# Kernel tuning notes

Measured on AMD Instinct MI355X. Metric: run time of the kernel, lower is better.

## Reference

```python
import jax, jax.numpy as jnp
import numpy as np

V, B, T, D, L, H = 32000, 2, 2048, 1024, 4, 16
HD = D // H            # 64
HID = int(2 * D * 4 / 3)  # 2730 (SwiGLU hidden, computed in BinaryMLP)
EPS = 1e-6


def setup_inputs() -> dict:
    key = jax.random.key(0)
    ks = jax.random.split(key, 16)
    s = 0.02
    return {
        'emb': jax.random.normal(ks[0], (V, D), jnp.float32) * s,
        'Wq':  jax.random.normal(ks[1], (L, D, D), jnp.float32) * s,
        'Wk':  jax.random.normal(ks[2], (L, D, D), jnp.float32) * s,
        'Wv':  jax.random.normal(ks[3], (L, D, D), jnp.float32) * s,
        'Wo':  jax.random.normal(ks[4], (L, D, D), jnp.float32) * s,
        'W1':  jax.random.normal(ks[5], (L, HID, D), jnp.float32) * s,
        'W3':  jax.random.normal(ks[6], (L, HID, D), jnp.float32) * s,
        'W2':  jax.random.normal(ks[7], (L, D, HID), jnp.float32) * s,
        'g1':  jnp.ones((L, D), jnp.float32),
        'g2':  jnp.ones((L, D), jnp.float32),
        'gf':  jnp.ones((D,), jnp.float32),
        'Wlm': jax.random.normal(ks[8], (V, D), jnp.float32) * s,
        'idx': jax.random.randint(ks[9], (B, T), 0, V, jnp.int64),
    }


def bitnet_quant(w):
    # BitNet b1.58: gamma = mean(|W|); ternarize then rescale (STE: identity grad)
    gamma = jnp.maximum(jnp.mean(jnp.abs(w)), 1e-5)
    wq = jnp.clip(jnp.round(w / gamma), -1.0, 1.0) * gamma
    return w + jax.lax.stop_gradient(wq - w)


def rmsnorm(x, g):
    return x * jax.lax.rsqrt(jnp.mean(x * x, axis=-1, keepdims=True) + EPS) * g


def rope_tables(t_len):
    inv_freq = 1.0 / (10000.0 ** (jnp.arange(0, HD, 2, dtype=jnp.float32) / HD))
    t = jnp.arange(t_len, dtype=jnp.float32)
    freqs = jnp.einsum('i,j->ij', t, inv_freq)       # [T, HD/2]
    emb = jnp.concatenate([freqs, freqs], axis=-1)    # [T, HD]
    return jnp.cos(emb), jnp.sin(emb)


def rotate_half(x):
    x1, x2 = x[..., : HD // 2], x[..., HD // 2:]
    return jnp.concatenate([-x2, x1], axis=-1)


def forward(emb, Wq, Wk, Wv, Wo, W1, W2, W3, g1, g2, gf, Wlm, idx):
    x = emb[idx]                                      # [B,T,D]
    cos, sin = rope_tables(T)                         # [T,HD]
    cos = cos[None, None]; sin = sin[None, None]      # [1,1,T,HD]
    causal = jnp.tril(jnp.ones((T, T), bool))[None, None]
    scale = 1.0 / np.sqrt(HD)

    for l in range(L):
        # --- attention ---
        h = rmsnorm(x, g1[l])
        q = jnp.einsum('btd,ed->bte', h, bitnet_quant(Wq[l]))
        k = jnp.einsum('btd,ed->bte', h, bitnet_quant(Wk[l]))
        v = jnp.einsum('btd,ed->bte', h, bitnet_quant(Wv[l]))
        q = q.reshape(B, T, H, HD).transpose(0, 2, 1, 3)  # [B,H,T,HD]
        k = k.reshape(B, T, H, HD).transpose(0, 2, 1, 3)
        v = v.reshape(B, T, H, HD).transpose(0, 2, 1, 3)
        q = q * cos + rotate_half(q) * sin
        k = k * cos + rotate_half(k) * sin
        att = jnp.einsum('bhqd,bhkd->bhqk', q, k) * scale
        att = jnp.where(causal, att, -jnp.inf)
        att = jax.nn.softmax(att, axis=-1)
        y = jnp.einsum('bhqk,bhkd->bhqd', att, v)
        y = y.transpose(0, 2, 1, 3).reshape(B, T, D)
        y = jnp.einsum('btd,ed->bte', y, bitnet_quant(Wo[l]))
        x = x + y
        # --- SwiGLU MLP ---
        h = rmsnorm(x, g2[l])
        a = jnp.einsum('btd,hd->bth', h, bitnet_quant(W1[l]))
        b = jnp.einsum('btd,hd->bth', h, bitnet_quant(W3[l]))
        m = jnp.einsum('bth,dh->btd', jax.nn.silu(a) * b, bitnet_quant(W2[l]))
        x = x + m

    x = rmsnorm(x, gf)
    logits = jnp.einsum('btd,vd->btv', x, Wlm)        # lm_head is plain Linear
    return logits


def reference(emb, Wq, Wk, Wv, Wo, W1, W2, W3, g1, g2, gf, Wlm, idx):
    return forward(emb, Wq, Wk, Wv, Wo, W1, W2, W3, g1, g2, gf, Wlm, idx)
```

## Files before the change

kernel.cpp:

```cpp
#include <hip/hip_runtime.h>

#define TT   2048
#define BBB  2
#define DDD  1024
#define LLL  4
#define HHH  16
#define VVV  32000
#define HIDR 2730
#define HIDP 2816
#define MMM  (BBB*TT)

typedef __bf16 bf16x8 __attribute__((ext_vector_type(8)));
typedef float  f32x4  __attribute__((ext_vector_type(4)));

#define BAR()    asm volatile("s_barrier" ::: "memory")
#define LGKM0()  asm volatile("s_waitcnt lgkmcnt(0)" ::: "memory")
#define VMC(n)   asm volatile("s_waitcnt vmcnt(" #n ")" ::: "memory")
#define SCHED0() __builtin_amdgcn_sched_barrier(0)

__device__ __forceinline__ void gl2lds16(const void* g, void* l) {
  __builtin_amdgcn_global_load_lds((const __attribute__((address_space(1))) void*)g,
                                   (__attribute__((address_space(3))) void*)l, 16, 0, 0);
}

__device__ __forceinline__ f32x4 mfma16(bf16x8 a, bf16x8 b, f32x4 c) {
  return __builtin_amdgcn_mfma_f32_16x16x32_bf16(a, b, c, 0, 0, 0);
}

__device__ __forceinline__ float block_reduce_sum(float v) {
  __shared__ float red[4];
  #pragma unroll
  for (int o = 32; o > 0; o >>= 1) v += __shfl_xor(v, o);
  int w = threadIdx.x >> 6;
  if ((threadIdx.x & 63) == 0) red[w] = v;
  __syncthreads();
  float r = red[0] + red[1] + red[2] + red[3];
  __syncthreads();
  return r;
}

struct QDesc { const float* src; __bf16* dst; int srcR, srcC, dstR, dstC, quant, rmul; };
struct QDescs { QDesc d[29]; };

__global__ __launch_bounds__(256) void reduce_abs_kernel(QDescs qd, float* partial) {
  const QDesc e = qd.d[blockIdx.y];
  size_t n4 = ((size_t)e.srcR * e.srcC) >> 2;
  const float4* s4 = (const float4*)e.src;
  float acc = 0.f;
  for (size_t i = (size_t)blockIdx.x * blockDim.x + threadIdx.x; i < n4;
       i += (size_t)gridDim.x * blockDim.x) {
    float4 v = s4[i];
    acc += fabsf(v.x) + fabsf(v.y) + fabsf(v.z) + fabsf(v.w);
  }
  float s = block_reduce_sum(acc);
  if (threadIdx.x == 0) partial[blockIdx.y * 256 + blockIdx.x] = s;
}

__global__ __launch_bounds__(256) void finalize_gamma_kernel(QDescs qd, const float* partial,
                                                             float* gamma) {
  int m = blockIdx.x;
  float v = partial[m * 256 + threadIdx.x];
  float s = block_reduce_sum(v);
  if (threadIdx.x == 0) {
    float n = (float)((size_t)qd.d[m].srcR * qd.d[m].srcC);
    gamma[m] = fmaxf(s / n, 1e-5f);
  }
}

__global__ __launch_bounds__(256) void quant_kernel(QDescs qd, const float* gamma) {
  const QDesc e = qd.d[blockIdx.y];
  float invg = 1.0f / gamma[blockIdx.y];
  int nc8 = e.dstC >> 3;
  for (int row = blockIdx.x; row < e.dstR; row += gridDim.x) {
    const float* srow = e.src + (size_t)row * e.srcC;
    bf16x8* drow = (bf16x8*)(e.dst + (size_t)row * e.rmul * e.dstC);
    bool rok = row < e.srcR;
    for (int c8 = threadIdx.x; c8 < nc8; c8 += 256) {
      int c = c8 * 8;
      float w[8];
      if (rok && c + 8 <= e.srcC) {
        float2 v01 = *(const float2*)(srow + c);
        float2 v23 = *(const float2*)(srow + c + 2);
        float2 v45 = *(const float2*)(srow + c + 4);
        float2 v67 = *(const float2*)(srow + c + 6);
        w[0] = v01.x; w[1] = v01.y; w[2] = v23.x; w[3] = v23.y;
        w[4] = v45.x; w[5] = v45.y; w[6] = v67.x; w[7] = v67.y;
      } else {
        #pragma unroll
        for (int j = 0; j < 8; ++j) w[j] = (rok && c + j < e.srcC) ? srow[c + j] : 0.f;
      }
      bf16x8 o;
      #pragma unroll
      for (int j = 0; j < 8; ++j) {
        if (e.quant) {
          float q = rintf(w[j] * invg);
          o[j] = (__bf16)fminf(1.f, fmaxf(-1.f, q));
        } else {
          o[j] = (__bf16)w[j];
        }
      }
      drow[c8] = o;
    }
  }
}

__global__ void rope_table_kernel(float* cosT, float* sinT) {
  int i = blockIdx.x * 256 + threadIdx.x;
  int t = i >> 5, j = i & 31;
  float inv = powf(10000.0f, -(float)j * (1.0f / 32.0f));
  float ang = (float)t * inv;
  cosT[i] = cosf(ang);
  sinT[i] = sinf(ang);
}

__global__ void idx_mode_kernel(const void* idxv, int* flag) {
  const long long* p = (const long long*)idxv;
  int good = 1;
  for (int i = threadIdx.x; i < (BBB * TT) / 2; i += 256) {
    long long v = p[i];
    if (v < 0 || v >= VVV) good = 0;
  }
  unsigned long long b = __ballot(good);
  __shared__ int r[4];
  if ((threadIdx.x & 63) == 0) r[threadIdx.x >> 6] = (b == ~0ULL) ? 1 : 0;
  __syncthreads();
  if (threadIdx.x == 0) flag[0] = r[0] & r[1] & r[2] & r[3];
}

__global__ __launch_bounds__(256) void gather_kernel(const float* emb, const void* idxv,
                                                     const int* flag, float* x) {
  int tok = blockIdx.x;
  long long id;
  if (flag[0]) id = ((const long long*)idxv)[tok];
  else         id = (long long)((const int*)idxv)[tok];
  const float4* src = (const float4*)(emb + (size_t)id * DDD);
  float4* dst = (float4*)(x + (size_t)tok * DDD);
  dst[threadIdx.x] = src[threadIdx.x];
}

__global__ __launch_bounds__(256) void rmsnorm_kernel(const float* x, const float* g, __bf16* h) {
  int tok = blockIdx.x;
  const float4* xr = (const float4*)(x + (size_t)tok * DDD);
  float4 v = xr[threadIdx.x];
  float ss = v.x * v.x + v.y * v.y + v.z * v.z + v.w * v.w;
  float tot = block_reduce_sum(ss);
  float r = rsqrtf(tot * (1.0f / (float)DDD) + 1e-6f);
  const float4* gr = (const float4*)g;
  float4 gv = gr[threadIdx.x];
  union { __bf16 o[4]; uint2 u2; } pk;
  pk.o[0] = (__bf16)(v.x * r * gv.x);
  pk.o[1] = (__bf16)(v.y * r * gv.y);
  pk.o[2] = (__bf16)(v.z * r * gv.z);
  pk.o[3] = (__bf16)(v.w * r * gv.w);
  *(uint2*)((char*)h + ((size_t)tok * DDD + threadIdx.x * 4) * 2) = pk.u2;
}

__global__ __launch_bounds__(256) void repack_kernel(const __bf16* qkv, const float* cosT,
                                                     const float* sinT, __bf16* Qp, __bf16* Kp,
                                                     __bf16* Vp) {
  int bh = blockIdx.y;
  int b = bh >> 4, h = bh & 15;
  int t0 = blockIdx.x * 64;
  int r = threadIdx.x >> 2;
  int cq = (threadIdx.x & 3) * 16;
  int t = t0 + r;
  __shared__ __bf16 vt[64][72];
  size_t src = ((size_t)b * TT + t) * 3072 + h * 64;

  #pragma unroll
  for (int which = 0; which < 2; ++which) {
    const __bf16* inp = qkv + (which ? 1024 : 0);
    __bf16* outp = which ? Kp : Qp;
    __bf16 val[16], par[16];
    *(bf16x8*)&val[0] = *(const bf16x8*)(inp + src + cq);
    *(bf16x8*)&val[8] = *(const bf16x8*)(inp + src + cq + 8);
    *(bf16x8*)&par[0] = *(const bf16x8*)(inp + src + (cq ^ 32));
    *(bf16x8*)&par[8] = *(const bf16x8*)(inp + src + (cq ^ 32) + 8);
    __bf16 o[16];
    #pragma unroll
    for (int i2 = 0; i2 < 16; ++i2) {
      int d = cq + i2;
      float c = cosT[t * 32 + (d & 31)];
      float s = sinT[t * 32 + (d & 31)];
      float x0 = (float)val[i2], xp = (float)par[i2];
      float res = (d < 32) ? (x0 * c - xp * s) : (x0 * c + xp * s);
      o[i2] = (__bf16)res;
    }
    *(bf16x8*)(outp + ((size_t)bh * TT + t) * 64 + cq) = *(bf16x8*)&o[0];
    *(bf16x8*)(outp + ((size_t)bh * TT + t) * 64 + cq + 8) = *(bf16x8*)&o[8];
  }

  bf16x8 v0 = *(const bf16x8*)(qkv + 2048 + src + cq);
  bf16x8 v1 = *(const bf16x8*)(qkv + 2048 + src + cq + 8);
  #pragma unroll
  for (int i2 = 0; i2 < 8; ++i2) {
    vt[r][cq + i2] = v0[i2];
    vt[r][cq + 8 + i2] = v1[i2];
  }
  __syncthreads();
  __bf16 ov[16];
  #pragma unroll
  for (int i2 = 0; i2 < 16; ++i2) ov[i2] = vt[cq + i2][r];
  *(bf16x8*)(Vp + ((size_t)bh * 64 + r) * TT + t0 + cq) = *(bf16x8*)&ov[0];
  *(bf16x8*)(Vp + ((size_t)bh * 64 + r) * TT + t0 + cq + 8) = *(bf16x8*)&ov[8];
}

__global__ __launch_bounds__(256) void attn_kernel(const __bf16* __restrict__ Qp,
                                                   const __bf16* __restrict__ Kp,
                                                   const __bf16* __restrict__ Vp,
                                                   __bf16* __restrict__ y) {
  int nwg = gridDim.x * gridDim.y;
  int orig = blockIdx.y * gridDim.x + blockIdx.x;
  int qq = nwg >> 3;
  int swz = (orig & 7) * qq + (orig >> 3);
  int qt = swz % gridDim.x, bh = swz / gridDim.x;

  int b = bh >> 4, h = bh & 15;
  int lane = threadIdx.x & 63, wave = threadIdx.x >> 6;
  int l15 = lane & 15, l4 = lane >> 4;
  int q0 = qt * 128;
  const int ssw = (l15 & 7);
  const int csw = ((lane & 7) ^ (lane >> 3)) * 8;
  const float SC = 0.125f * 1.44269504f;

  __shared__ __bf16 Ks[2][64 * 64];
  __shared__ __bf16 Vts[2][64 * 64];
  __shared__ __bf16 Ps[4][32 * 64];

  const __bf16* Qb = Qp + (size_t)bh * TT * 64;
  bf16x8 qf[2][2];
  #pragma unroll
  for (int mf = 0; mf < 2; ++mf)
    #pragma unroll
    for (int kk = 0; kk < 2; ++kk)
      qf[mf][kk] = *(const bf16x8*)(Qb + (size_t)(q0 + wave * 32 + mf * 16 + l15) * 64 +
                                    kk * 32 + l4 * 8);

  const f32x4 z4 = {0.f, 0.f, 0.f, 0.f};
  f32x4 acc[2][4];
  float mrow[2][4], lrow[2][4];
  #pragma unroll
  for (int mf = 0; mf < 2; ++mf)
    #pragma unroll
    for (int j = 0; j < 4; ++j) { mrow[mf][j] = -1e30f; lrow[mf][j] = 0.f; }
  #pragma unroll
  for (int mf = 0; mf < 2; ++mf)
    #pragma unroll
    for (int df = 0; df < 4; ++df) acc[mf][df] = z4;

  auto stage = [&](int kt, int buf) {
    int k0 = kt * 64;
    #pragma unroll
    for (int i = 0; i < 2; ++i) {
      int rbase = wave * 16 + i * 8;
      int row = rbase + (lane >> 3);
      gl2lds16(Kp + ((size_t)bh * TT + k0 + row) * 64 + csw, &Ks[buf][rbase * 64]);
      gl2lds16(Vp + ((size_t)bh * 64 + row) * TT + k0 + csw, &Vts[buf][rbase * 64]);
    }
  };

  int nkt = q0 / 64 + 2;
  stage(0, 0);
  __syncthreads();

  for (int kt = 0; kt < nkt; ++kt) {
    int k0 = kt * 64;
    int cur = kt & 1;
    if (kt + 1 < nkt) stage(kt + 1, cur ^ 1);
    const __bf16* KsC = Ks[cur];
    const __bf16* VtsC = Vts[cur];

    f32x4 s[2][4];
    #pragma unroll
    for (int mf = 0; mf < 2; ++mf)
      #pragma unroll
      for (int nf = 0; nf < 4; ++nf) s[mf][nf] = z4;
    __builtin_amdgcn_s_setprio(1);
    #pragma unroll
    for (int kk = 0; kk < 2; ++kk) {
      int slot = ((kk * 4 + l4) ^ ssw) * 8;
      bf16x8 kf[4];
      #pragma unroll
      for (int nf = 0; nf < 4; ++nf)
        kf[nf] = *(const bf16x8*)&KsC[(nf * 16 + l15) * 64 + slot];
      #pragma unroll
      for (int mf = 0; mf < 2; ++mf)
        #pragma unroll
        for (int nf = 0; nf < 4; ++nf) s[mf][nf] = mfma16(qf[mf][kk], kf[nf], s[mf][nf]);
    }
    __builtin_amdgcn_s_setprio(0);

    bool domask = (k0 + 63 > q0);
    #pragma unroll
    for (int mf = 0; mf < 2; ++mf) {
      int qrowb = q0 + wave * 32 + mf * 16 + l4 * 4;
      #pragma unroll
      for (int nf = 0; nf < 4; ++nf) {
        int kg = k0 + nf * 16 + l15;
        #pragma unroll
        for (int j = 0; j < 4; ++j) {
          float vv = s[mf][nf][j] * SC;
          if (domask && kg > qrowb + j) vv = -1e30f;
          s[mf][nf][j] = vv;
        }
      }
    }

    float mx_[2][4];
    float exm = -1e30f;
    #pragma unroll
    for (int mf = 0; mf < 2; ++mf)
      #pragma unroll
      for (int j = 0; j < 4; ++j) {
        float mx = fmaxf(fmaxf(s[mf][0][j], s[mf][1][j]), fmaxf(s[mf][2][j], s[mf][3][j]));
        mx = fmaxf(mx, __shfl_xor(mx, 1));
        mx = fmaxf(mx, __shfl_xor(mx, 2));
        mx = fmaxf(mx, __shfl_xor(mx, 4));
        mx = fmaxf(mx, __shfl_xor(mx, 8));
        mx_[mf][j] = mx;
        exm = fmaxf(exm, mx - mrow[mf][j]);
      }
    if (__ballot(exm > 8.0f) != 0ULL) {
      #pragma unroll
      for (int mf = 0; mf < 2; ++mf)
        #pragma unroll
        for (int j = 0; j < 4; ++j) {
          float mnew = fmaxf(mrow[mf][j], mx_[mf][j]);
          float alpha = exp2f(mrow[mf][j] - mnew);
          mrow[mf][j] = mnew;
          lrow[mf][j] *= alpha;
          #pragma unroll
          for (int df = 0; df < 4; ++df) acc[mf][df][j] *= alpha;
        }
    }

    float psum[2][4];
    #pragma unroll
    for (int mf = 0; mf < 2; ++mf)
      #pragma unroll
      for (int j = 0; j < 4; ++j) psum[mf][j] = 0.f;
    #pragma unroll
    for (int mf = 0; mf < 2; ++mf)
      #pragma unroll
      for (int nf = 0; nf < 4; ++nf)
        #pragma unroll
        for (int j = 0; j < 4; ++j) {
          float pp = exp2f(s[mf][nf][j] - mrow[mf][j]);
          psum[mf][j] += pp;
          int prow = mf * 16 + l4 * 4 + j;
          int pcol = nf * 16 + l15;
          Ps[wave][prow * 64 + (pcol ^ ((prow & 7) << 3))] = (__bf16)pp;
        }
    #pragma unroll
    for (int mf = 0; mf < 2; ++mf)
      #pragma unroll
      for (int j = 0; j < 4; ++j) {
        float rs = psum[mf][j];
        rs += __shfl_xor(rs, 1);
        rs += __shfl_xor(rs, 2);
        rs += __shfl_xor(rs, 4);
        rs += __shfl_xor(rs, 8);
        lrow[mf][j] += rs;
      }

    __builtin_amdgcn_s_setprio(1);
    #pragma unroll
    for (int kk = 0; kk < 2; ++kk) {
      int slot = ((kk * 4 + l4) ^ ssw) * 8;
      bf16x8 pf[2], vf[4];
      #pragma unroll
      for (int mf = 0; mf < 2; ++mf)
        pf[mf] = *(const bf16x8*)&Ps[wave][(mf * 16 + l15) * 64 + slot];
      #pragma unroll
      for (int df = 0; df < 4; ++df)
        vf[df] = *(const bf16x8*)&VtsC[(df * 16 + l15) * 64 + slot];
      #pragma unroll
      for (int mf = 0; mf < 2; ++mf)
        #pragma unroll
        for (int df = 0; df < 4; ++df) acc[mf][df] = mfma16(pf[mf], vf[df], acc[mf][df]);
    }
    __builtin_amdgcn_s_setprio(0);
    __syncthreads();
  }

  #pragma unroll
  for (int mf = 0; mf < 2; ++mf)
    #pragma unroll
    for (int j = 0; j < 4; ++j) {
      float inv = 1.0f / lrow[mf][j];
      int qg = q0 + wave * 32 + mf * 16 + l4 * 4 + j;
      size_t base = ((size_t)b * TT + qg) * DDD + h * 64;
      #pragma unroll
      for (int df = 0; df < 4; ++df)
        y[base + df * 16 + l15] = (__bf16)(acc[mf][df][j] * inv);
    }
}

template <int MODE>
__global__ __launch_bounds__(256) void gemm_kernel(const __bf16* __restrict__ A,
                                                   const __bf16* __restrict__ Bw, void* Cout,
                                                   const float* Res, const float* gscale,
                                                   int gshift, int M, int N, int K) {
  __shared__ __bf16 As[128 * 64];
  __shared__ __bf16 Bs[128 * 64];
  int nwg = gridDim.x * gridDim.y;
  int orig = blockIdx.y * gridDim.x + blockIdx.x;
  int qq = nwg >> 3;
  int swz = (orig & 7) * qq + (orig >> 3);
  int bx = swz % gridDim.x, by = swz / gridDim.x;
  const int m0 = bx * 128, n0 = by * 128;

  const int lane = threadIdx.x & 63, wave = threadIdx.x >> 6;
  const int wr = wave >> 1, wc = wave & 1;
  const int l15 = lane & 15, l4 = lane >> 4;
  const int ssw = (l15 & 7);
  const int csw = ((lane & 7) ^ (lane >> 3)) * 8;
  const f32x4 z4 = {0.f, 0.f, 0.f, 0.f};
  f32x4 acc[4][4];
  #pragma unroll
  for (int i = 0; i < 4; ++i)
    #pragma unroll
    for (int j = 0; j < 4; ++j) acc[i][j] = z4;

  const int nk = K >> 6;
  for (int kt = 0; kt < nk; ++kt) {
    const int kb = kt << 6;
    #pragma unroll
    for (int i = 0; i < 4; ++i) {
      int rbase = wave * 32 + i * 8;
      int row = rbase + (lane >> 3);
      gl2lds16(A + (size_t)(m0 + row) * K + kb + csw, &As[rbase * 64]);
      gl2lds16(Bw + (size_t)(n0 + row) * K + kb + csw, &Bs[rbase * 64]);
    }
    __syncthreads();
    #pragma unroll
    for (int kk = 0; kk < 2; ++kk) {
      int slot = ((kk * 4 + l4) ^ ssw) * 8;
      bf16x8 af[4], bfr[4];
      #pragma unroll
      for (int mi = 0; mi < 4; ++mi)
        af[mi] = *(const bf16x8*)&As[(wr * 64 + mi * 16 + l15) * 64 + slot];
      #pragma unroll
      for (int ni = 0; ni < 4; ++ni)
        bfr[ni] = *(const bf16x8*)&Bs[(wc * 64 + ni * 16 + l15) * 64 + slot];
      #pragma unroll
      for (int mi = 0; mi < 4; ++mi)
        #pragma unroll
        for (int ni = 0; ni < 4; ++ni) acc[mi][ni] = mfma16(af[mi], bfr[ni], acc[mi][ni]);
    }
    __syncthreads();
  }

  float sc = gscale ? gscale[n0 >> gshift] : 1.0f;
  #pragma unroll
  for (int mi = 0; mi < 4; ++mi)
    #pragma unroll
    for (int ni = 0; ni < 4; ++ni)
      #pragma unroll
      for (int j = 0; j < 4; ++j) {
        int r = m0 + wr * 64 + mi * 16 + l4 * 4 + j;
        int c = n0 + wc * 64 + ni * 16 + l15;
        size_t off = (size_t)r * N + c;
        float v = acc[mi][ni][j] * sc;
        if (MODE == 0) ((__bf16*)Cout)[off] = (__bf16)v;
        else if (MODE == 1) ((float*)Cout)[off] = Res[off] + v;
        else ((float*)Cout)[off] = v;
      }
}

template <int MODE>
__global__ __launch_bounds__(512, 2) void gemm256_kernel(const __bf16* __restrict__ A,
                                                         const __bf16* __restrict__ Bw,
                                                         void* Cout, const float* Res,
                                                         const float* gscale, int gshift,
                                                         int M, int N, int K) {
  __shared__ __bf16 AS[2][2][256 * 32];
  __shared__ __bf16 BS[2][2][256 * 32];
  int nwg = gridDim.x * gridDim.y;
  int orig = blockIdx.y * gridDim.x + blockIdx.x;
  int qq = nwg >> 3;
  int swz = (orig & 7) * qq + (orig >> 3);
  int bx = swz % gridDim.x, by = swz / gridDim.x;
  const int m0 = bx * 256, n0 = by * 256;

  const int tid = threadIdx.x;
  const int lane = tid & 63, w = tid >> 6;
  const int wr = w >> 2, wc = w & 3;
  const int l15 = lane & 15, l4 = lane >> 4;
  const int lsw = (l15 >> 1) & 3;
  const int srow = w * 16 + (lane >> 2);
  const int sslot = ((lane & 3) ^ ((lane >> 3) & 3)) * 8;

  f32x4 acc[8][4];
  const f32x4 z4 = {0.f, 0.f, 0.f, 0.f};
  #pragma unroll
  for (int i = 0; i < 8; ++i)
    #pragma unroll
    for (int j = 0; j < 4; ++j) acc[i][j] = z4;

  auto stageA = [&](int b, int kh, int t) {
    const __bf16* g = A + (size_t)(m0 + srow) * K + (size_t)t * 64 + kh * 32 + sslot;
    gl2lds16(g, &AS[b][kh][w * 512]);
    gl2lds16(g + (size_t)128 * K, &AS[b][kh][4096 + w * 512]);
  };
  auto stageB = [&](int b, int kh, int t) {
    const __bf16* g = Bw + (size_t)(n0 + srow) * K + (size_t)t * 64 + kh * 32 + sslot;
    gl2lds16(g, &BS[b][kh][w * 512]);
    gl2lds16(g + (size_t)128 * K, &BS[b][kh][4096 + w * 512]);
  };

  bf16x8 af[4], bq[4];
  auto ldA = [&](int b, int kh, int mh) {
    #pragma unroll
    for (int mi = 0; mi < 4; ++mi) {
      int row = wr * 128 + (mh * 4 + mi) * 16 + l15;
      af[mi] = *(const bf16x8*)&AS[b][kh][row * 32 + ((l4 ^ lsw) * 8)];
    }
  };
  auto ldB = [&](int b, int kh) {
    #pragma unroll
    for (int ni = 0; ni < 4; ++ni) {
      int row = wc * 64 + ni * 16 + l15;
      bq[ni] = *(const bf16x8*)&BS[b][kh][row * 32 + ((l4 ^ lsw) * 8)];
    }
  };
  auto domfma = [&](int mh) {
    __builtin_amdgcn_s_setprio(1);
    #pragma unroll
    for (int mi = 0; mi < 4; ++mi)
      #pragma unroll
      for (int ni = 0; ni < 4; ++ni)
        acc[mh * 4 + mi][ni] = mfma16(af[mi], bq[ni], acc[mh * 4 + mi][ni]);
    __builtin_amdgcn_s_setprio(0);
  };

  const int nk = K >> 6;
  const int niter = nk >> 1;
  stageA(0, 0, 0); stageB(0, 0, 0); stageA(0, 1, 0); stageB(0, 1, 0);
  stageB(1, 0, 1); stageA(1, 0, 1); stageB(1, 1, 1);
  VMC(6); SCHED0();
  BAR();

  for (int j = 0; j < niter; ++j) {
    int t1 = 2 * j + 1;
    int t2 = 2 * j + 2; if (t2 > nk - 1) t2 = nk - 1;
    int t3 = 2 * j + 3; if (t3 > nk - 1) t3 = nk - 1;
    ldB(0, 0); ldA(0, 0, 0);
    stageA(1, 1, t1);
    BAR(); LGKM0(); SCHED0();
    domfma(0);
    BAR();
    ldA(0, 0, 1);
    stageB(0, 0, t2);
    BAR(); LGKM0(); SCHED0();
    domfma(1);
    BAR();
    ldB(0, 1); ldA(0, 1, 0);
    stageA(0, 0, t2);
    BAR(); LGKM0(); SCHED0();
    domfma(0);
    BAR();
    ldA(0, 1, 1);
    VMC(4); SCHED0();
    stageB(0, 1, t2);
    BAR(); LGKM0(); SCHED0();
    domfma(1);
    BAR();
    ldB(1, 0); ldA(1, 0, 0);
    stageA(0, 1, t2);
    BAR(); LGKM0(); SCHED0();
    domfma(0);
    BAR();
    ldA(1, 0, 1);
    stageB(1, 0, t3);
    BAR(); LGKM0(); SCHED0();
    domfma(1);
    BAR();
    ldB(1, 1); ldA(1, 1, 0);
    stageA(1, 0, t3);
    BAR(); LGKM0(); SCHED0();
    domfma(0);
    BAR();
    ldA(1, 1, 1);
    VMC(4); SCHED0();
    stageB(1, 1, t3);
    BAR(); LGKM0(); SCHED0();
    domfma(1);
    BAR();
  }

  if (MODE == 3) {
    float g1v = gscale[0], g3v = gscale[4];
    __bf16* U = (__bf16*)Cout;
    int half = N >> 1;
    #pragma unroll
    for (int mi = 0; mi < 8; ++mi)
      #pragma unroll
      for (int ni = 0; ni < 4; ++ni)
        #pragma unroll
        for (int j = 0; j < 4; ++j) {
          int r = m0 + wr * 128 + mi * 16 + l4 * 4 + j;
          int c = n0 + wc * 64 + ni * 16 + l15;
          float v = acc[mi][ni][j];
          float av = v * g1v;
          float bv = v * g3v;
          float pav = __shfl_xor(av, 1);
          float pbv = __shfl_xor(bv, 1);
          float aa = (lane & 1) ? pav : av;
          float bb = (lane & 1) ? bv : pbv;
          float u = aa / (1.0f + __expf(-aa)) * bb;
          if (!(lane & 1)) U[(size_t)r * half + (c >> 1)] = (__bf16)u;
        }
    return;
  }

  float sc = gscale ? gscale[n0 >> gshift] : 1.0f;
  #pragma unroll
  for (int mi = 0; mi < 8; ++mi)
    #pragma unroll
    for (int ni = 0; ni < 4; ++ni)
      #pragma unroll
      for (int j = 0; j < 4; ++j) {
        int r = m0 + wr * 128 + mi * 16 + l4 * 4 + j;
        int c = n0 + wc * 64 + ni * 16 + l15;
        size_t off = (size_t)r * N + c;
        float v = acc[mi][ni][j] * sc;
        if (MODE == 0) ((__bf16*)Cout)[off] = (__bf16)v;
        else if (MODE == 1) ((float*)Cout)[off] = Res[off] + v;
        else ((float*)Cout)[off] = v;
      }
}

extern "C" void kernel_launch(void* const* d_in, const int* in_sizes, int n_in,
                              void* d_out, int out_size, void* d_ws, size_t ws_size,
                              hipStream_t stream) {
  (void)in_sizes; (void)n_in; (void)out_size; (void)ws_size;
  const float* emb = (const float*)d_in[0];
  const float* Wq  = (const float*)d_in[1];
  const float* Wk  = (const float*)d_in[2];
  const float* Wv  = (const float*)d_in[3];
  const float* Wo  = (const float*)d_in[4];
  const float* W1  = (const float*)d_in[5];
  const float* W3  = (const float*)d_in[6];
  const float* W2  = (const float*)d_in[7];
  const float* g1  = (const float*)d_in[8];
  const float* g2  = (const float*)d_in[9];
  const float* gf  = (const float*)d_in[10];
  const float* Wlm = (const float*)d_in[11];
  const void*  idx = d_in[12];
  float* out = (float*)d_out;

  char* p = (char*)d_ws;
  auto take = [&](size_t bytes) -> char* {
    char* r = p;
    p += (bytes + 255) & ~(size_t)255;
    return r;
  };
  __bf16* WqkvQ = (__bf16*)take((size_t)LLL * 3072 * DDD * 2);
  __bf16* WoQ  = (__bf16*)take((size_t)LLL * DDD * DDD * 2);
  __bf16* W13Q = (__bf16*)take((size_t)LLL * 2 * HIDP * DDD * 2);
  __bf16* W2Q  = (__bf16*)take((size_t)LLL * DDD * HIDP * 2);
  __bf16* WlmB = (__bf16*)take((size_t)VVV * DDD * 2);
  float*  xbuf = (float*)take((size_t)MMM * DDD * 4);
  __bf16* hbuf = (__bf16*)take((size_t)MMM * DDD * 2);
  char*   S    = take(69206016);
  float*  cosT = (float*)take((size_t)TT * 32 * 4);
  float*  sinT = (float*)take((size_t)TT * 32 * 4);
  float*  gamma = (float*)take(128);
  float*  partial = (float*)take(29 * 256 * 4);
  int*    flag = (int*)take(256);

  __bf16* qkv = (__bf16*)(S);
  __bf16* Qp  = (__bf16*)(S + 25165824);
  __bf16* Kp  = (__bf16*)(S + 33554432);
  __bf16* Vp  = (__bf16*)(S + 41943040);
  __bf16* ub  = (__bf16*)(S + 46137344);

  QDescs qd;
  for (int l = 0; l < LLL; ++l) {
    qd.d[l * 4 + 0] = QDesc{Wq + (size_t)l * DDD * DDD,
                            WqkvQ + (size_t)l * 3072 * DDD, DDD, DDD, DDD, DDD, 1, 1};
    qd.d[l * 4 + 1] = QDesc{Wk + (size_t)l * DDD * DDD,
                            WqkvQ + (size_t)l * 3072 * DDD + (size_t)DDD * DDD,
                            DDD, DDD, DDD, DDD, 1, 1};
    qd.d[l * 4 + 2] = QDesc{Wv + (size_t)l * DDD * DDD,
                            WqkvQ + (size_t)l * 3072 * DDD + (size_t)2 * DDD * DDD,
                            DDD, DDD, DDD, DDD, 1, 1};
    qd.d[l * 4 + 3] = QDesc{Wo + (size_t)l * DDD * DDD, WoQ + (size_t)l * DDD * DDD,
                            DDD, DDD, DDD, DDD, 1, 1};
    qd.d[16 + l] = QDesc{W1 + (size_t)l * HIDR * DDD,
                         W13Q + (size_t)l * 2 * HIDP * DDD,
                         HIDR, DDD, HIDP, DDD, 1, 2};
    qd.d[20 + l] = QDesc{W3 + (size_t)l * HIDR * DDD,
                         W13Q + (size_t)l * 2 * HIDP * DDD + (size_t)DDD,
                         HIDR, DDD, HIDP, DDD, 1, 2};
    qd.d[24 + l] = QDesc{W2 + (size_t)l * DDD * HIDR, W2Q + (size_t)l * DDD * HIDP,
                         DDD, HIDR, DDD, HIDP, 1, 1};
  }
  qd.d[28] = QDesc{Wlm, WlmB, VVV, DDD, VVV, DDD, 0, 1};

  reduce_abs_kernel<<<dim3(256, 28), 256, 0, stream>>>(qd, partial);
  finalize_gamma_kernel<<<28, 256, 0, stream>>>(qd, partial, gamma);
  quant_kernel<<<dim3(512, 29), 256, 0, stream>>>(qd, gamma);
  rope_table_kernel<<<(TT * 32) / 256, 256, 0, stream>>>(cosT, sinT);
  idx_mode_kernel<<<1, 256, 0, stream>>>(idx, flag);
  gather_kernel<<<MMM, 256, 0, stream>>>(emb, idx, flag, xbuf);

  for (int l = 0; l < LLL; ++l) {
    rmsnorm_kernel<<<MMM, 256, 0, stream>>>(xbuf, g1 + (size_t)l * DDD, hbuf);
    gemm256_kernel<0><<<dim3(16, 12), 512, 0, stream>>>(
        hbuf, WqkvQ + (size_t)l * 3072 * DDD, qkv, nullptr, gamma + l * 4, 10,
        MMM, 3072, DDD);
    repack_kernel<<<dim3(TT / 64, BBB * HHH), 256, 0, stream>>>(qkv, cosT, sinT, Qp, Kp, Vp);
    attn_kernel<<<dim3(TT / 128, BBB * HHH), 256, 0, stream>>>(Qp, Kp, Vp, hbuf);
    gemm_kernel<1><<<dim3(32, 8), 256, 0, stream>>>(hbuf, WoQ + (size_t)l * DDD * DDD, xbuf,
                                                    xbuf, gamma + l * 4 + 3, 30, MMM, DDD, DDD);
    rmsnorm_kernel<<<MMM, 256, 0, stream>>>(xbuf, g2 + (size_t)l * DDD, hbuf);
    gemm256_kernel<3><<<dim3(16, 2 * HIDP / 256), 512, 0, stream>>>(
        hbuf, W13Q + (size_t)l * 2 * HIDP * DDD, ub, nullptr, gamma + 16 + l, 30,
        MMM, 2 * HIDP, DDD);
    gemm_kernel<1><<<dim3(32, 8), 256, 0, stream>>>(ub, W2Q + (size_t)l * DDD * HIDP, xbuf,
                                                    xbuf, gamma + 24 + l, 30, MMM, DDD, HIDP);
  }
  rmsnorm_kernel<<<MMM, 256, 0, stream>>>(xbuf, gf, hbuf);
  gemm256_kernel<2><<<dim3(16, VVV / 256), 512, 0, stream>>>(hbuf, WlmB, out, nullptr, nullptr,
                                                             30, MMM, VVV, DDD);
}
```

Before: 2.007 ms.

## Restructure GEMM main loop into four coarse phases with full A fragment loads

Replaces the eight fine-grained sub-phases per iteration with four phases. Each phase loads both halves of the A fragments and the B fragments, issues one A and one B stage, and runs all 32 MFMAs. This halves the number of barriers and LDS waits per k-tile, which should cut synchronization overhead. In exchange it holds more fragment registers (af0 and af1), has less fine-grained interleaving of loads with MFMAs, and changes the vmcnt accounting in the prologue and each phase.

```diff
diff --git a/kernel.cpp b/kernel.cpp
--- a/kernel.cpp
+++ b/kernel.cpp
@@ -509,12 +509,17 @@
     gl2lds16(g + (size_t)128 * K, &BS[b][kh][4096 + w * 512]);
   };
 
-  bf16x8 af[4], bq[4];
-  auto ldA = [&](int b, int kh, int mh) {
+  bf16x8 af0[4], af1[4], bq[4];
+  auto ldA2 = [&](int b, int kh) {
     #pragma unroll
     for (int mi = 0; mi < 4; ++mi) {
-      int row = wr * 128 + (mh * 4 + mi) * 16 + l15;
-      af[mi] = *(const bf16x8*)&AS[b][kh][row * 32 + ((l4 ^ lsw) * 8)];
+      int row0 = wr * 128 + mi * 16 + l15;
+      af0[mi] = *(const bf16x8*)&AS[b][kh][row0 * 32 + ((l4 ^ lsw) * 8)];
+    }
+    #pragma unroll
+    for (int mi = 0; mi < 4; ++mi) {
+      int row1 = wr * 128 + (4 + mi) * 16 + l15;
+      af1[mi] = *(const bf16x8*)&AS[b][kh][row1 * 32 + ((l4 ^ lsw) * 8)];
     }
   };
   auto ldB = [&](int b, int kh) {
@@ -524,70 +529,48 @@
       bq[ni] = *(const bf16x8*)&BS[b][kh][row * 32 + ((l4 ^ lsw) * 8)];
     }
   };
-  auto domfma = [&](int mh) {
+  auto domfma2 = [&]() {
     __builtin_amdgcn_s_setprio(1);
     #pragma unroll
     for (int mi = 0; mi < 4; ++mi)
       #pragma unroll
       for (int ni = 0; ni < 4; ++ni)
-        acc[mh * 4 + mi][ni] = mfma16(af[mi], bq[ni], acc[mh * 4 + mi][ni]);
+        acc[mi][ni] = mfma16(af0[mi], bq[ni], acc[mi][ni]);
+    #pragma unroll
+    for (int mi = 0; mi < 4; ++mi)
+      #pragma unroll
+      for (int ni = 0; ni < 4; ++ni)
+        acc[4 + mi][ni] = mfma16(af1[mi], bq[ni], acc[4 + mi][ni]);
     __builtin_amdgcn_s_setprio(0);
   };
+
+#define PHASE(bb, kh, sb, skh, st)                                                \
+  {                                                                               \
+    ldB(bb, kh); ldA2(bb, kh);                                                    \
+    stageA(sb, skh, st); stageB(sb, skh, st);                                     \
+    BAR(); LGKM0(); SCHED0();                                                     \
+    domfma2();                                                                    \
+    VMC(8); SCHED0();                                                             \
+    BAR();                                                                        \
+  }
 
   const int nk = K >> 6;
   const int niter = nk >> 1;
   stageA(0, 0, 0); stageB(0, 0, 0); stageA(0, 1, 0); stageB(0, 1, 0);
-  stageB(1, 0, 1); stageA(1, 0, 1); stageB(1, 1, 1);
-  VMC(6); SCHED0();
+  stageA(1, 0, 1); stageB(1, 0, 1);
+  VMC(4); SCHED0();
   BAR();
 
   for (int j = 0; j < niter; ++j) {
     int t1 = 2 * j + 1;
     int t2 = 2 * j + 2; if (t2 > nk - 1) t2 = nk - 1;
     int t3 = 2 * j + 3; if (t3 > nk - 1) t3 = nk - 1;
-    ldB(0, 0); ldA(0, 0, 0);
-    stageA(1, 1, t1);
-    BAR(); LGKM0(); SCHED0();
-    domfma(0);
-    BAR();
-    ldA(0, 0, 1);
-    stageB(0, 0, t2);
-    BAR(); LGKM0(); SCHED0();
-    domfma(1);
-    BAR();
-    ldB(0, 1); ldA(0, 1, 0);
-    stageA(0, 0, t2);
-    BAR(); LGKM0(); SCHED0();
-    domfma(0);
-    BAR();
-    ldA(0, 1, 1);
-    VMC(4); SCHED0();
-    stageB(0, 1, t2);
-    BAR(); LGKM0(); SCHED0();
-    domfma(1);
-    BAR();
-    ldB(1, 0); ldA(1, 0, 0);
-    stageA(0, 1, t2);
-    BAR(); LGKM0(); SCHED0();
-    domfma(0);
-    BAR();
-    ldA(1, 0, 1);
-    stageB(1, 0, t3);
-    BAR(); LGKM0(); SCHED0();
-    domfma(1);
-    BAR();
-    ldB(1, 1); ldA(1, 1, 0);
-    stageA(1, 0, t3);
-    BAR(); LGKM0(); SCHED0();
-    domfma(0);
-    BAR();
-    ldA(1, 1, 1);
-    VMC(4); SCHED0();
-    stageB(1, 1, t3);
-    BAR(); LGKM0(); SCHED0();
-    domfma(1);
-    BAR();
-  }
+    PHASE(0, 0, 1, 1, t1);
+    PHASE(0, 1, 0, 0, t2);
+    PHASE(1, 0, 0, 1, t2);
+    PHASE(1, 1, 1, 0, t3);
+  }
+#undef PHASE
 
   if (MODE == 3) {
     float g1v = gscale[0], g3v = gscale[4];
```

Measured after the change: 2.080 ms. +3.6%, slower.
